# Kernel tuning notes

Measured on AMD Instinct MI355X. Metric: run time of the kernel, lower is better.

Reference implementation:

```python
import jax, jax.numpy as jnp
import numpy as np

TARGET_FIDELITY = 0.95
WEIGHT = 0.1
BATCH, DIM = 8192, 2048


def setup_inputs() -> dict:
    key = jax.random.key(0)
    k1, k2 = jax.random.split(key)
    # Scale by 1/sqrt(DIM) so each row is roughly unit-norm (quantum-state-like)
    # and the trace fidelity lands strictly inside the clamp interval [0, 1].
    scale = 1.0 / np.sqrt(DIM)
    latent_codes = jax.random.normal(k1, (BATCH, DIM), dtype=jnp.float32) * scale
    target_codes = jax.random.normal(k2, (BATCH, DIM), dtype=jnp.float32) * scale
    return {"latent_codes": latent_codes, "target_codes": target_codes}


def reference(latent_codes, target_codes):
    batch = latent_codes.shape[0]
    # rho = mean_i z_i z_i^T  ==  L^T L / B  (single GEMM instead of B outer products)
    rho = jnp.matmul(latent_codes.T, latent_codes) / batch      # [D, D]
    sigma = jnp.matmul(target_codes.T, target_codes) / batch    # [D, D]
    # trace(rho @ sigma) = sum(rho * sigma) since both are symmetric
    fidelity = jnp.clip(jnp.sum(rho * sigma), 0.0, 1.0)
    loss = WEIGHT * jnp.abs(fidelity - TARGET_FIDELITY)
    return loss
```

## Files before the change

### kernel.cpp

```cpp
#include <hip/hip_runtime.h>
#include <stdint.h>

#define BATCH 8192
#define DIM   2048
#define NT    272
#define QTOT  (NT * 32)
#define QPB   17
#define NSLOT 768

typedef unsigned char  u8;
typedef unsigned short u16;
typedef unsigned int   u32;

using v8i   = __attribute__((ext_vector_type(8)))  int;
using v16f  = __attribute__((ext_vector_type(16))) float;
using f32x4 = __attribute__((ext_vector_type(4)))  float;

#if __has_builtin(__builtin_amdgcn_cvt_scalef32_pk_fp4_f32)
#define HW_FP4 1
#endif

__device__ __forceinline__ void gl_lds16(const void* g, void* l) {
  __builtin_amdgcn_global_load_lds(
      (const __attribute__((address_space(1))) u32*)g,
      (__attribute__((address_space(3))) u32*)l, 16, 0, 0);
}

__device__ __forceinline__ int piece_base(int b) {
  const int m = b & 31;
  const int p = (m <= 16) ? (m >> 1) : (8 + ((m - 15) >> 1));
  return b + 16 * (b >> 5) + p;
}

__device__ __forceinline__ u32 nib4(float x) {
  float xs = x * 64.0f;
  float a  = fabsf(xs);
  u32 n = (u32)(a >= 0.25f) + (u32)(a >= 0.75f) + (u32)(a >= 1.25f) +
          (u32)(a >= 1.75f) + (u32)(a >= 2.5f)  + (u32)(a >= 3.5f)  +
          (u32)(a >= 5.0f);
  return n | (xs < 0.0f ? 8u : 0u);
}

__device__ __forceinline__ u16 pack4_fp4(float a, float b, float c, float d) {
#ifdef HW_FP4
  u32 w = __builtin_amdgcn_cvt_scalef32_pk_fp4_f32(0u,  a * 64.0f, b * 64.0f, 1.0f, 0);
  w     = __builtin_amdgcn_cvt_scalef32_pk_fp4_f32(w,   c * 64.0f, d * 64.0f, 1.0f, 1);
  return (u16)w;
#else
  return (u16)(nib4(a) | (nib4(b) << 4) | (nib4(c) << 8) | (nib4(d) << 12));
#endif
}

__global__ __launch_bounds__(256) void tcvt_fp4(
    const float* __restrict__ L, const float* __restrict__ T,
    u8* __restrict__ X, u8* __restrict__ Y,
    float* __restrict__ acc, u32* __restrict__ cnt)
{
  __shared__ u16 ls[64 * 68];

  const int tid = threadIdx.x;
  if (blockIdx.x == 0 && tid == 0) { *acc = 0.0f; *cnt = 0u; }

  int id = blockIdx.x;
  const float* src;
  u8* dst;
  if (id < 1024) { src = L; dst = X; }
  else           { src = T; dst = Y; id -= 1024; }
  const int d0 = (id & 31) * 64;
  const int b0 = (id >> 5) * 256;

  const int s  = tid & 15;
  const int g  = tid >> 4;
  const int sw = s & 12;

  const float* base = src + (size_t)(b0 + g * 4) * DIM + d0 + s * 4;

  f32x4 f[2][4];
#pragma unroll
  for (int r = 0; r < 4; ++r)
    f[0][r] = *(const f32x4*)(base + (size_t)r * DIM);

#pragma unroll
  for (int j = 0; j < 4; ++j) {
    if (j < 3) {
#pragma unroll
      for (int r = 0; r < 4; ++r)
        f[(j + 1) & 1][r] = *(const f32x4*)(base + (size_t)((j + 1) * 64 + r) * DIM);
    }
    const int w = (j * 16 + g) ^ sw;
#pragma unroll
    for (int i = 0; i < 4; ++i)
      ls[(s * 4 + i) * 68 + w] =
          pack4_fp4(f[j & 1][0][i], f[j & 1][1][i], f[j & 1][2][i], f[j & 1][3][i]);
  }
  __syncthreads();

#pragma unroll
  for (int j2 = 0; j2 < 2; ++j2) {
    const int d   = (tid >> 3) + j2 * 32;
    const int o8  = tid & 7;
    const int gsw = (d >> 4) & 3;
    const int g1  = (2 * o8)     ^ gsw;
    const int g2  = (2 * o8 + 1) ^ gsw;
    uint2 a = *(const uint2*)&ls[d * 68 + g1 * 4];
    uint2 b = *(const uint2*)&ls[d * 68 + g2 * 4];
    uint4 v = {a.x, a.y, b.x, b.y};
    *(uint4*)(dst + (size_t)(d0 + d) * (BATCH / 2) + (b0 >> 1) + o8 * 16) = v;
  }
}

__global__ __launch_bounds__(256, 2) void gram_fp4(
    const u8* __restrict__ X, const u8* __restrict__ Y,
    float* __restrict__ P)
{
  __shared__ u8 ls[2][2][16384];

  const int tid = threadIdx.x;
  const int bid = blockIdx.x;

  const int wave = tid >> 6;
  const int lane = tid & 63;
  const int wr = (wave >> 1) * 64;
  const int wc = (wave & 1) * 64;
  const int lr = lane & 31;
  const int kh = lane >> 5;

  u32 sdst[4]; int srow[4], sgc16[4];
#pragma unroll
  for (int rr = 0; rr < 4; ++rr) {
    const int li  = rr * 256 + tid;
    const int row = li >> 3;
    const int p   = li & 7;
    sdst[rr]  = (u32)(row * 128 + p * 16);
    srow[rr]  = row;
    sgc16[rr] = (p ^ (row & 7)) * 16;
  }

  u32 fa[2][4], fb[2][4];
#pragma unroll
  for (int h = 0; h < 2; ++h) {
    const int ra = wr + h * 32 + lr;
    const int rb = wc + h * 32 + lr;
#pragma unroll
    for (int ks = 0; ks < 4; ++ks) {
      const int c = 2 * ks + kh;
      fa[h][ks] = (u32)(ra * 128 + (c ^ (ra & 7)) * 16);
      fb[h][ks] = (u32)(rb * 128 + (c ^ (rb & 7)) * 16);
    }
  }

  v16f acc[2][2] = {};
  const int sc = 0x7F7F7F7F;

  const int q0  = bid * QPB;
  const int t0b = q0 >> 5;
  const int sl0 = piece_base(bid);
  int cur_t = -1, buf = 0;
  const u8* src = X;
  u32 soi[4], soj[4];

  for (int it = 0; it < QPB; ++it) {
    const int q = q0 + it;
    const int t = q >> 5;
    const int k = q & 31;

    if (t != cur_t) {
      const int ltile = (t < 136) ? t : t - 136;
      src = (t < 136) ? X : Y;
      int ti = 0;
      while ((ti + 1) * (ti + 2) / 2 <= ltile) ++ti;
      const int tj = ltile - ti * (ti + 1) / 2;
      const int i0 = ti * 128;
      const int j0 = tj * 128;
#pragma unroll
      for (int rr = 0; rr < 4; ++rr) {
        soi[rr] = (u32)(i0 + srow[rr]) * (BATCH / 2) + sgc16[rr];
        soj[rr] = (u32)(j0 + srow[rr]) * (BATCH / 2) + sgc16[rr];
      }
      const u32 kb = (u32)k * 128;
#pragma unroll
      for (int rr = 0; rr < 4; ++rr) {
        gl_lds16(src + soi[rr] + kb, &ls[buf][0][sdst[rr]]);
        gl_lds16(src + soj[rr] + kb, &ls[buf][1][sdst[rr]]);
      }
      if (cur_t >= 0) {
        float4* o = (float4*)(P + (size_t)(sl0 + (cur_t - t0b)) * 16384);
#pragma unroll
        for (int h = 0; h < 2; ++h)
#pragma unroll
          for (int hc = 0; hc < 2; ++hc)
#pragma unroll
            for (int r4 = 0; r4 < 4; ++r4) {
              float4 v = {acc[h][hc][r4 * 4 + 0], acc[h][hc][r4 * 4 + 1],
                          acc[h][hc][r4 * 4 + 2], acc[h][hc][r4 * 4 + 3]};
              o[((h * 2 + hc) * 4 + r4) * 256 + tid] = v;
            }
#pragma unroll
        for (int h = 0; h < 2; ++h)
#pragma unroll
          for (int hc = 0; hc < 2; ++hc)
#pragma unroll
            for (int c2 = 0; c2 < 16; ++c2)
              acc[h][hc][c2] = 0.0f;
      }
      cur_t = t;
    }

    __syncthreads();
    if (it + 1 < QPB && ((q + 1) >> 5) == t) {
      const u32 kb = (u32)(k + 1) * 128;
#pragma unroll
      for (int rr = 0; rr < 4; ++rr) {
        gl_lds16(src + soi[rr] + kb, &ls[buf ^ 1][0][sdst[rr]]);
        gl_lds16(src + soj[rr] + kb, &ls[buf ^ 1][1][sdst[rr]]);
      }
    }

    const u8* pI = ls[buf][0];
    const u8* pJ = ls[buf][1];
#pragma unroll
    for (int ks = 0; ks < 4; ++ks) {
      v8i a[2], b[2];
#pragma unroll
      for (int h = 0; h < 2; ++h) {
        int4 pa = *(const int4*)&pI[fa[h][ks]];
        a[h] = (v8i){pa.x, pa.y, pa.z, pa.w, 0, 0, 0, 0};
        int4 pb = *(const int4*)&pJ[fb[h][ks]];
        b[h] = (v8i){pb.x, pb.y, pb.z, pb.w, 0, 0, 0, 0};
      }
#pragma unroll
      for (int h = 0; h < 2; ++h)
#pragma unroll
        for (int hc = 0; hc < 2; ++hc)
          acc[h][hc] = __builtin_amdgcn_mfma_scale_f32_32x32x64_f8f6f4(
              a[h], b[hc], acc[h][hc],  4,  4,
              0, sc, 0, sc);
    }
    buf ^= 1;
  }

  {
    float4* o = (float4*)(P + (size_t)(sl0 + (cur_t - t0b)) * 16384);
#pragma unroll
    for (int h = 0; h < 2; ++h)
#pragma unroll
      for (int hc = 0; hc < 2; ++hc)
#pragma unroll
        for (int r4 = 0; r4 < 4; ++r4) {
          float4 v = {acc[h][hc][r4 * 4 + 0], acc[h][hc][r4 * 4 + 1],
                      acc[h][hc][r4 * 4 + 2], acc[h][hc][r4 * 4 + 3]};
          o[((h * 2 + hc) * 4 + r4) * 256 + tid] = v;
        }
  }
}

__device__ __forceinline__ int collect_pieces(int t, int* s) {
  const int qlo = 32 * t, qhi = 32 * t + 31;
  const int b_lo = qlo / 17, b_hi = qhi / 17;
  int n = 0;
  for (int b = b_lo; b <= b_hi; ++b) {
    const int tfirst = (17 * b) >> 5;
    s[n++] = piece_base(b) + (t - tfirst);
  }
  return n;
}

__global__ __launch_bounds__(256) void dot_kernel(
    const float4* __restrict__ P4,
    float* __restrict__ d_acc, u32* __restrict__ d_cnt,
    float* __restrict__ out)
{
  __shared__ float red[4];
  const int tid  = threadIdx.x;
  const int lane = tid & 63;
  const int lt   = blockIdx.x >> 1;
  const int half = blockIdx.x & 1;

  int ti = 0;
  while ((ti + 1) * (ti + 2) / 2 <= lt) ++ti;
  const int tj = lt - ti * (ti + 1) / 2;
  const float w = (ti == tj) ? 1.0f : 2.0f;

  int sx[3], sy[3];
  const int nx = collect_pieces(lt, sx);
  const int ny = collect_pieces(136 + lt, sy);

  const size_t ho = (size_t)half * 2048;
  float s = 0.0f;
#pragma unroll
  for (int j = 0; j < 8; ++j) {
    const int e = tid + j * 256;
    float4 a = P4[(size_t)sx[0] * 4096 + ho + e];
    {
      float4 u = P4[(size_t)sx[1] * 4096 + ho + e];
      a.x += u.x; a.y += u.y; a.z += u.z; a.w += u.w;
    }
    if (nx == 3) {
      float4 u = P4[(size_t)sx[2] * 4096 + ho + e];
      a.x += u.x; a.y += u.y; a.z += u.z; a.w += u.w;
    }
    float4 b = P4[(size_t)sy[0] * 4096 + ho + e];
    {
      float4 u = P4[(size_t)sy[1] * 4096 + ho + e];
      b.x += u.x; b.y += u.y; b.z += u.z; b.w += u.w;
    }
    if (ny == 3) {
      float4 u = P4[(size_t)sy[2] * 4096 + ho + e];
      b.x += u.x; b.y += u.y; b.z += u.z; b.w += u.w;
    }
    s += a.x * b.x + a.y * b.y + a.z * b.z + a.w * b.w;
  }
  s *= w;
#pragma unroll
  for (int off = 32; off > 0; off >>= 1)
    s += __shfl_down(s, off);
  if (lane == 0) red[tid >> 6] = s;
  __syncthreads();
  if (tid == 0) {
    atomicAdd(d_acc, red[0] + red[1] + red[2] + red[3]);
    __threadfence();
    const u32 old = atomicAdd(d_cnt, 1u);
    if (old == 271u) {
      float S   = atomicAdd(d_acc, 0.0f);
      float fid = S * 0x1.0p-50f;
      fid = fminf(fmaxf(fid, 0.0f), 1.0f);
      *out = 0.1f * fabsf(fid - 0.95f);
    }
  }
}

extern "C" void kernel_launch(void* const* d_in, const int* in_sizes, int n_in,
                              void* d_out, int out_size, void* d_ws, size_t ws_size,
                              hipStream_t stream) {
  const float* L = (const float*)d_in[0];
  const float* T = (const float*)d_in[1];
  float* out = (float*)d_out;

  const size_t NF4 = (size_t)BATCH * DIM / 2;
  u8*    X   = (u8*)d_ws;
  u8*    Y   = (u8*)d_ws + NF4;
  float* P   = (float*)((char*)d_ws + 2 * NF4);
  float* acc = P + (size_t)NSLOT * 16384;
  u32*   cnt = (u32*)(acc + 1);

  tcvt_fp4<<<2048, 256, 0, stream>>>(L, T, X, Y, acc, cnt);
  gram_fp4<<<512, 256, 0, stream>>>(X, Y, P);
  dot_kernel<<<272, 256, 0, stream>>>((const float4*)P, acc, cnt, out);
}
```

Before: 199.9 us.

## Load all rows upfront, skip duplicate diag tile loads, remap blocks, widen dot grid

The transpose-convert kernel now issues all sixteen row loads up front instead of double-buffering them, which raises memory-level parallelism at the cost of more registers. In the gram kernel, diagonal tiles load only the I panel and reuse it for J, halving global-to-LDS traffic for those tiles. Block IDs are permuted (interleaved by 8), presumably to spread work or cache locality across XCDs. The final dot kernel launches 2176 single-chunk blocks instead of 272 blocks looping over 8 chunks, which improves occupancy but multiplies the global atomics.

```diff
diff --git a/kernel.cpp b/kernel.cpp
--- a/kernel.cpp
+++ b/kernel.cpp
@@ -7,6 +7,7 @@
 #define QTOT  (NT * 32)
 #define QPB   17
 #define NSLOT 768
+#define DOTBLK (136 * 16)
 
 typedef unsigned char  u8;
 typedef unsigned short u16;
@@ -14,7 +15,6 @@
 
 using v8i   = __attribute__((ext_vector_type(8)))  int;
 using v16f  = __attribute__((ext_vector_type(16))) float;
-using f32x4 = __attribute__((ext_vector_type(4)))  float;
 
 #if __has_builtin(__builtin_amdgcn_cvt_scalef32_pk_fp4_f32)
 #define HW_FP4 1
@@ -73,25 +73,22 @@
   const int g  = tid >> 4;
   const int sw = s & 12;
 
-  const float* base = src + (size_t)(b0 + g * 4) * DIM + d0 + s * 4;
-
-  f32x4 f[2][4];
-#pragma unroll
-  for (int r = 0; r < 4; ++r)
-    f[0][r] = *(const f32x4*)(base + (size_t)r * DIM);
+  float4 f[4][4];
+#pragma unroll
+  for (int j = 0; j < 4; ++j)
+#pragma unroll
+    for (int r = 0; r < 4; ++r)
+      f[j][r] = *(const float4*)(src + (size_t)(b0 + j * 64 + g * 4 + r) * DIM
+                                 + d0 + s * 4);
 
 #pragma unroll
   for (int j = 0; j < 4; ++j) {
-    if (j < 3) {
-#pragma unroll
-      for (int r = 0; r < 4; ++r)
-        f[(j + 1) & 1][r] = *(const f32x4*)(base + (size_t)((j + 1) * 64 + r) * DIM);
-    }
     const int w = (j * 16 + g) ^ sw;
+    const float* fp[4] = {(const float*)&f[j][0], (const float*)&f[j][1],
+                          (const float*)&f[j][2], (const float*)&f[j][3]};
 #pragma unroll
     for (int i = 0; i < 4; ++i)
-      ls[(s * 4 + i) * 68 + w] =
-          pack4_fp4(f[j & 1][0][i], f[j & 1][1][i], f[j & 1][2][i], f[j & 1][3][i]);
+      ls[(s * 4 + i) * 68 + w] = pack4_fp4(fp[0][i], fp[1][i], fp[2][i], fp[3][i]);
   }
   __syncthreads();
 
@@ -116,7 +113,7 @@
   __shared__ u8 ls[2][2][16384];
 
   const int tid = threadIdx.x;
-  const int bid = blockIdx.x;
+  const int bid = ((blockIdx.x & 7) << 6) | (blockIdx.x >> 3);
 
   const int wave = tid >> 6;
   const int lane = tid & 63;
@@ -156,6 +153,7 @@
   const int t0b = q0 >> 5;
   const int sl0 = piece_base(bid);
   int cur_t = -1, buf = 0;
+  bool diag = false;
   const u8* src = X;
   u32 soi[4], soj[4];
 
@@ -172,6 +170,7 @@
       const int tj = ltile - ti * (ti + 1) / 2;
       const int i0 = ti * 128;
       const int j0 = tj * 128;
+      diag = (ti == tj);
 #pragma unroll
       for (int rr = 0; rr < 4; ++rr) {
         soi[rr] = (u32)(i0 + srow[rr]) * (BATCH / 2) + sgc16[rr];
@@ -179,10 +178,12 @@
       }
       const u32 kb = (u32)k * 128;
 #pragma unroll
-      for (int rr = 0; rr < 4; ++rr) {
+      for (int rr = 0; rr < 4; ++rr)
         gl_lds16(src + soi[rr] + kb, &ls[buf][0][sdst[rr]]);
-        gl_lds16(src + soj[rr] + kb, &ls[buf][1][sdst[rr]]);
-      }
+      if (!diag)
+#pragma unroll
+        for (int rr = 0; rr < 4; ++rr)
+          gl_lds16(src + soj[rr] + kb, &ls[buf][1][sdst[rr]]);
       if (cur_t >= 0) {
         float4* o = (float4*)(P + (size_t)(sl0 + (cur_t - t0b)) * 16384);
 #pragma unroll
@@ -210,14 +211,16 @@
     if (it + 1 < QPB && ((q + 1) >> 5) == t) {
       const u32 kb = (u32)(k + 1) * 128;
 #pragma unroll
-      for (int rr = 0; rr < 4; ++rr) {
+      for (int rr = 0; rr < 4; ++rr)
         gl_lds16(src + soi[rr] + kb, &ls[buf ^ 1][0][sdst[rr]]);
-        gl_lds16(src + soj[rr] + kb, &ls[buf ^ 1][1][sdst[rr]]);
-      }
+      if (!diag)
+#pragma unroll
+        for (int rr = 0; rr < 4; ++rr)
+          gl_lds16(src + soj[rr] + kb, &ls[buf ^ 1][1][sdst[rr]]);
     }
 
     const u8* pI = ls[buf][0];
-    const u8* pJ = ls[buf][1];
+    const u8* pJ = diag ? ls[buf][0] : ls[buf][1];
 #pragma unroll
     for (int ks = 0; ks < 4; ++ks) {
       v8i a[2], b[2];
@@ -273,8 +276,8 @@
   __shared__ float red[4];
   const int tid  = threadIdx.x;
   const int lane = tid & 63;
-  const int lt   = blockIdx.x >> 1;
-  const int half = blockIdx.x & 1;
+  const int lt   = blockIdx.x >> 4;
+  const int ch   = blockIdx.x & 15;
 
   int ti = 0;
   while ((ti + 1) * (ti + 2) / 2 <= lt) ++ti;
@@ -285,32 +288,27 @@
   const int nx = collect_pieces(lt, sx);
   const int ny = collect_pieces(136 + lt, sy);
 
-  const size_t ho = (size_t)half * 2048;
-  float s = 0.0f;
-#pragma unroll
-  for (int j = 0; j < 8; ++j) {
-    const int e = tid + j * 256;
-    float4 a = P4[(size_t)sx[0] * 4096 + ho + e];
-    {
-      float4 u = P4[(size_t)sx[1] * 4096 + ho + e];
-      a.x += u.x; a.y += u.y; a.z += u.z; a.w += u.w;
-    }
-    if (nx == 3) {
-      float4 u = P4[(size_t)sx[2] * 4096 + ho + e];
-      a.x += u.x; a.y += u.y; a.z += u.z; a.w += u.w;
-    }
-    float4 b = P4[(size_t)sy[0] * 4096 + ho + e];
-    {
-      float4 u = P4[(size_t)sy[1] * 4096 + ho + e];
-      b.x += u.x; b.y += u.y; b.z += u.z; b.w += u.w;
-    }
-    if (ny == 3) {
-      float4 u = P4[(size_t)sy[2] * 4096 + ho + e];
-      b.x += u.x; b.y += u.y; b.z += u.z; b.w += u.w;
-    }
-    s += a.x * b.x + a.y * b.y + a.z * b.z + a.w * b.w;
-  }
-  s *= w;
+  const int e = ch * 256 + tid;
+  float4 a = P4[(size_t)sx[0] * 4096 + e];
+  {
+    float4 u = P4[(size_t)sx[1] * 4096 + e];
+    a.x += u.x; a.y += u.y; a.z += u.z; a.w += u.w;
+  }
+  if (nx == 3) {
+    float4 u = P4[(size_t)sx[2] * 4096 + e];
+    a.x += u.x; a.y += u.y; a.z += u.z; a.w += u.w;
+  }
+  float4 b = P4[(size_t)sy[0] * 4096 + e];
+  {
+    float4 u = P4[(size_t)sy[1] * 4096 + e];
+    b.x += u.x; b.y += u.y; b.z += u.z; b.w += u.w;
+  }
+  if (ny == 3) {
+    float4 u = P4[(size_t)sy[2] * 4096 + e];
+    b.x += u.x; b.y += u.y; b.z += u.z; b.w += u.w;
+  }
+  float s = (a.x * b.x + a.y * b.y + a.z * b.z + a.w * b.w) * w;
+
 #pragma unroll
   for (int off = 32; off > 0; off >>= 1)
     s += __shfl_down(s, off);
@@ -320,7 +318,7 @@
     atomicAdd(d_acc, red[0] + red[1] + red[2] + red[3]);
     __threadfence();
     const u32 old = atomicAdd(d_cnt, 1u);
-    if (old == 271u) {
+    if (old == (u32)(DOTBLK - 1)) {
       float S   = atomicAdd(d_acc, 0.0f);
       float fid = S * 0x1.0p-50f;
       fid = fminf(fmaxf(fid, 0.0f), 1.0f);
@@ -345,5 +343,5 @@
 
   tcvt_fp4<<<2048, 256, 0, stream>>>(L, T, X, Y, acc, cnt);
   gram_fp4<<<512, 256, 0, stream>>>(X, Y, P);
-  dot_kernel<<<272, 256, 0, stream>>>((const float4*)P, acc, cnt, out);
-}
+  dot_kernel<<<DOTBLK, 256, 0, stream>>>((const float4*)P, acc, cnt, out);
+}
```

Measured after the change: 245.8 us. 1.23x slower.
